# Optimization experiments

Measured on AMD Instinct MI355X. Metric: run time of the kernel, lower is better.

The kernel has to match this reference:

```python
import jax, jax.numpy as jnp
import numpy as np

HID, NH, HD = 1024, 16, 64
WIN = 512
DFF, NE, TOPK = 4096, 8, 2
B, S = 1, 2048
EPS = 1e-6


def _rope_rotation_matrix(seq_len, head_dim):
    # Block-diagonal 2x2 rotation matrices per position (standard RoPE as a fused matrix).
    pos = np.arange(seq_len, dtype=np.float64)
    inv_freq = 1.0 / (10000.0 ** (np.arange(0, head_dim, 2, dtype=np.float64) / head_dim))
    ang = pos[:, None] * inv_freq[None, :]            # [S, HD/2]
    c, s = np.cos(ang), np.sin(ang)
    R = np.zeros((seq_len, head_dim, head_dim), np.float32)
    i = np.arange(0, head_dim, 2)
    R[:, i, i] = c
    R[:, i + 1, i + 1] = c
    R[:, i, i + 1] = -s
    R[:, i + 1, i] = s
    return jnp.asarray(R)


def setup_inputs() -> dict:
    key = jax.random.key(0)
    ks = jax.random.split(key, 10)
    init = lambda k, shape, scale=0.02: (jax.random.normal(k, shape, jnp.float32) * scale)
    return {
        "x": jax.random.normal(ks[0], (B, S, HID), jnp.float32),
        "rotation_matrix": _rope_rotation_matrix(S, HD),
        "rms1_w": jnp.ones((HID,), jnp.float32),
        "wq": init(ks[1], (HID, HID)),
        "wk": init(ks[2], (HID, HID)),
        "wv": init(ks[3], (HID, HID)),
        "wo": init(ks[4], (HID, HID)),
        "rms2_w": jnp.ones((HID,), jnp.float32),
        "gate_w": init(ks[5], (HID, NE)),
        "w1": init(ks[6], (NE, HID, DFF)),
        "w2": init(ks[7], (NE, DFF, HID)),
        "w3": init(ks[8], (NE, HID, DFF)),
    }


def _rmsnorm(x, w):
    return x * jax.lax.rsqrt(jnp.mean(x * x, axis=-1, keepdims=True) + EPS) * w


def reference(x, rotation_matrix, rms1_w, wq, wk, wv, wo, rms2_w, gate_w, w1, w2, w3):
    b, s, _ = x.shape
    # --- sliding-window attention with fused RoPE rotation matrix ---
    y = _rmsnorm(x, rms1_w)
    q = (y @ wq).reshape(b, s, NH, HD).transpose(0, 2, 1, 3)  # bhsd
    k = (y @ wk).reshape(b, s, NH, HD).transpose(0, 2, 1, 3)
    v = (y @ wv).reshape(b, s, NH, HD).transpose(0, 2, 1, 3)
    q = jnp.einsum('bhsd,sde->bhse', q, rotation_matrix)
    k = jnp.einsum('bhsd,sde->bhse', k, rotation_matrix)
    scores = jnp.einsum('bhqd,bhkd->bhqk', q, k) / np.float32(np.sqrt(HD))
    idx = jnp.arange(s)
    mask = (idx[:, None] >= idx[None, :]) & (idx[:, None] - idx[None, :] < WIN)
    scores = jnp.where(mask[None, None], scores, jnp.float32(-1e9))
    att = jax.nn.softmax(scores, axis=-1)
    attn_out = jnp.einsum('bhqk,bhkd->bhqd', att, v)
    attn_out = attn_out.transpose(0, 2, 1, 3).reshape(b, s, HID) @ wo
    x = x + attn_out
    # --- MoE SwiGLU FFN with top-k routing ---
    y = _rmsnorm(x, rms2_w)
    t = y.reshape(b * s, HID)                                  # [T, D]
    logits = t @ gate_w                                        # [T, E]
    top_v, top_i = jax.lax.top_k(logits, TOPK)
    gates = jax.nn.softmax(top_v, axis=-1)                     # [T, K]
    w_full = jnp.zeros((b * s, NE), t.dtype).at[
        jnp.arange(b * s)[:, None], top_i].set(gates)          # [T, E] sparse routing weights
    h = jax.nn.silu(jnp.einsum('td,edf->etf', t, w1)) * jnp.einsum('td,edf->etf', t, w3)
    expert_out = jnp.einsum('etf,efd->etd', h, w2)             # [E, T, D]
    moe = jnp.einsum('te,etd->td', w_full, expert_out).reshape(b, s, HID)
    return x + moe
```

## Files before the change

kernel.cpp:

```cpp
#include <hip/hip_runtime.h>
#include <hip/hip_bf16.h>
#include <stdint.h>


#define S_ 2048
#define HID_ 1024
#define NH_ 16
#define HD_ 64
#define WIN_ 512
#define DFF_ 4096
#define NE_ 8

typedef unsigned short u16;
typedef __attribute__((ext_vector_type(8))) short short8;
typedef __attribute__((ext_vector_type(4))) float f32x4;

__device__ __forceinline__ u16 f2bf(float f) {
  union { float f; unsigned u; } v; v.f = f;
  unsigned r = (v.u + 0x7FFFu + ((v.u >> 16) & 1u)) >> 16;
  return (u16)r;
}
__device__ __forceinline__ float bf2f(u16 b) {
  union { unsigned u; float f; } v; v.u = ((unsigned)b) << 16;
  return v.f;
}

__device__ __forceinline__ void gload16(const void* g, void* l) {
  __builtin_amdgcn_global_load_lds(
      (const __attribute__((address_space(1))) void*)g,
      (__attribute__((address_space(3))) void*)l, 16, 0, 0);
}

template <int N>
__device__ __forceinline__ void waitcnt_vm() {
  static_assert(N == 0 || N == 4 || N == 8 || N == 12 || N == 16 || N == 24,
                "unsupported vmcnt");
  if constexpr (N == 0) asm volatile("s_waitcnt vmcnt(0)" ::: "memory");
  else if constexpr (N == 4) asm volatile("s_waitcnt vmcnt(4)" ::: "memory");
  else if constexpr (N == 8) asm volatile("s_waitcnt vmcnt(8)" ::: "memory");
  else if constexpr (N == 12) asm volatile("s_waitcnt vmcnt(12)" ::: "memory");
  else if constexpr (N == 16) asm volatile("s_waitcnt vmcnt(16)" ::: "memory");
  else if constexpr (N == 24) asm volatile("s_waitcnt vmcnt(24)" ::: "memory");
}

__global__ __launch_bounds__(256) void convT_f32_k(const float* __restrict__ W,
                                                   u16* __restrict__ WT,
                                                   int K, int N, size_t matStride) {
  __shared__ u16 t[64][72];
  const float* Wm = W + (size_t)blockIdx.z * matStride;
  u16* WTm = WT + (size_t)blockIdx.z * matStride;
  int n0 = blockIdx.x * 64, k0 = blockIdx.y * 64;
  int tid = threadIdx.x;
  int cw = (tid & 15) * 4, rr = tid >> 4;
#pragma unroll
  for (int p = 0; p < 4; ++p) {
    int r = p * 16 + rr;
    float4 v = *(const float4*)&Wm[(size_t)(k0 + r) * N + n0 + cw];
    t[cw][r] = f2bf(v.x);
    t[cw + 1][r] = f2bf(v.y);
    t[cw + 2][r] = f2bf(v.z);
    t[cw + 3][r] = f2bf(v.w);
  }
  __syncthreads();
#pragma unroll
  for (int p = 0; p < 4; ++p) {
    int n = p * 16 + rr;
    ushort4 pk = *(const ushort4*)&t[n][cw];
    *(ushort4*)&WTm[(size_t)(n0 + n) * K + k0 + cw] = pk;
  }
}

__global__ __launch_bounds__(256) void convT_qkvo_k(const float* __restrict__ wq,
                                                    const float* __restrict__ wk,
                                                    const float* __restrict__ wv,
                                                    const float* __restrict__ wo,
                                                    u16* __restrict__ outT) {
  __shared__ u16 t[64][72];
  int z = blockIdx.z;
  const float* Wm = (z == 0) ? wq : (z == 1) ? wk : (z == 2) ? wv : wo;
  u16* WTm = outT + (size_t)z * HID_ * HID_;
  int n0 = blockIdx.x * 64, k0 = blockIdx.y * 64;
  int tid = threadIdx.x;
  int cw = (tid & 15) * 4, rr = tid >> 4;
#pragma unroll
  for (int p = 0; p < 4; ++p) {
    int r = p * 16 + rr;
    float4 v = *(const float4*)&Wm[(size_t)(k0 + r) * HID_ + n0 + cw];
    t[cw][r] = f2bf(v.x);
    t[cw + 1][r] = f2bf(v.y);
    t[cw + 2][r] = f2bf(v.z);
    t[cw + 3][r] = f2bf(v.w);
  }
  __syncthreads();
#pragma unroll
  for (int p = 0; p < 4; ++p) {
    int n = p * 16 + rr;
    ushort4 pk = *(const ushort4*)&t[n][cw];
    *(ushort4*)&WTm[(size_t)(n0 + n) * HID_ + k0 + cw] = pk;
  }
}

__global__ __launch_bounds__(256) void convT_u16_k(const u16* __restrict__ W,
                                                   u16* __restrict__ WT,
                                                   int K, int N, size_t matStride) {
  __shared__ u16 t[64][66];
  const u16* Wm = W + (size_t)blockIdx.z * matStride;
  u16* WTm = WT + (size_t)blockIdx.z * matStride;
  int n0 = blockIdx.x * 64, k0 = blockIdx.y * 64;
  int tid = threadIdx.x;
  int c2 = (tid & 31) * 2, rr = tid >> 5;
#pragma unroll
  for (int it = 0; it < 8; ++it) {
    int r = it * 8 + rr;
    unsigned vv = *(const unsigned*)&Wm[(size_t)(k0 + r) * N + n0 + c2];
    t[c2][r] = (u16)vv;
    t[c2 + 1][r] = (u16)(vv >> 16);
  }
  __syncthreads();
#pragma unroll
  for (int it = 0; it < 8; ++it) {
    int n = it * 8 + rr;
    unsigned pk = (unsigned)t[n][c2] | ((unsigned)t[n][c2 + 1] << 16);
    *(unsigned*)&WTm[(size_t)(n0 + n) * K + k0 + c2] = pk;
  }
}

__global__ __launch_bounds__(256) void rope_tab_k(const float* __restrict__ rot,
                                                  float* __restrict__ cost,
                                                  float* __restrict__ sint) {
  int id = blockIdx.x * 256 + threadIdx.x;
  if (id >= S_ * 32) return;
  int s = id >> 5, j = id & 31;
  cost[id] = rot[(size_t)s * 4096 + (size_t)(2 * j) * 64 + 2 * j];
  sint[id] = rot[(size_t)s * 4096 + (size_t)(2 * j + 1) * 64 + 2 * j];
}

__global__ __launch_bounds__(256) void rms1_k(const float* __restrict__ x,
                                              const float* __restrict__ rw,
                                              u16* __restrict__ y) {
  int row = blockIdx.x, tid = threadIdx.x;
  const float4 v = *(const float4*)&x[(size_t)row * HID_ + tid * 4];
  float ss = v.x * v.x + v.y * v.y + v.z * v.z + v.w * v.w;
#pragma unroll
  for (int o = 32; o; o >>= 1) ss += __shfl_xor(ss, o);
  __shared__ float red[4];
  if ((tid & 63) == 0) red[tid >> 6] = ss;
  __syncthreads();
  float rstd = rsqrtf((red[0] + red[1] + red[2] + red[3]) * (1.f / HID_) + 1e-6f);
  const float4 w4 = *(const float4*)&rw[tid * 4];
  ushort4 o4;
  o4.x = f2bf(v.x * rstd * w4.x);
  o4.y = f2bf(v.y * rstd * w4.y);
  o4.z = f2bf(v.z * rstd * w4.z);
  o4.w = f2bf(v.w * rstd * w4.w);
  *(ushort4*)&y[(size_t)row * HID_ + tid * 4] = o4;
}

__global__ __launch_bounds__(256) void rms2_gate_k(const float* __restrict__ x2,
                                                   const float* __restrict__ rw,
                                                   const float* __restrict__ gw,
                                                   u16* __restrict__ y2,
                                                   float* __restrict__ logits) {
  int row = blockIdx.x, tid = threadIdx.x;
  int wv = tid >> 6, ln = tid & 63;
  const float4 v = *(const float4*)&x2[(size_t)row * HID_ + tid * 4];
  float ss = v.x * v.x + v.y * v.y + v.z * v.z + v.w * v.w;
#pragma unroll
  for (int o = 32; o; o >>= 1) ss += __shfl_xor(ss, o);
  __shared__ float red[4];
  __shared__ float lred[4][8];
  if (ln == 0) red[wv] = ss;
  __syncthreads();
  float rstd = rsqrtf((red[0] + red[1] + red[2] + red[3]) * (1.f / HID_) + 1e-6f);
  const float4 w4 = *(const float4*)&rw[tid * 4];
  float yv[4];
  yv[0] = v.x * rstd * w4.x; yv[1] = v.y * rstd * w4.y;
  yv[2] = v.z * rstd * w4.z; yv[3] = v.w * rstd * w4.w;
  ushort4 o4;
  o4.x = f2bf(yv[0]); o4.y = f2bf(yv[1]); o4.z = f2bf(yv[2]); o4.w = f2bf(yv[3]);
  *(ushort4*)&y2[(size_t)row * HID_ + tid * 4] = o4;
  float le[8] = {0, 0, 0, 0, 0, 0, 0, 0};
  int d0 = tid * 4;
#pragma unroll
  for (int j = 0; j < 4; ++j) {
    const float* grow = &gw[(size_t)(d0 + j) * NE_];
#pragma unroll
    for (int e = 0; e < 8; ++e) le[e] += yv[j] * grow[e];
  }
#pragma unroll
  for (int e = 0; e < 8; ++e) {
    float t = le[e];
#pragma unroll
    for (int o = 32; o; o >>= 1) t += __shfl_xor(t, o);
    le[e] = t;
  }
  if (ln == 0)
#pragma unroll
    for (int e = 0; e < 8; ++e) lred[wv][e] = le[e];
  __syncthreads();
  if (tid < 8)
    logits[(size_t)row * NE_ + tid] =
        lred[0][tid] + lred[1][tid] + lred[2][tid] + lred[3][tid];
}

__global__ __launch_bounds__(1024) void route_k(const float* __restrict__ logits,
                                                int* __restrict__ topi,
                                                float* __restrict__ topg,
                                                int* __restrict__ counts,
                                                int* __restrict__ ebase,
                                                int* __restrict__ slot_token,
                                                int* __restrict__ slot_of) {
  __shared__ int cnt[8], bas[8], rnk[8];
  int tid = threadIdx.x;
  if (tid < 8) { cnt[tid] = 0; rnk[tid] = 0; }
  __syncthreads();
  int e0[2], e1[2];
  float g0[2], g1[2];
#pragma unroll
  for (int s = 0; s < 2; ++s) {
    int t = tid * 2 + s;
    const float* lg = &logits[(size_t)t * NE_];
    float v0 = -1e30f; int i0 = 0;
#pragma unroll
    for (int e = 0; e < 8; ++e) {
      float x = lg[e];
      if (x > v0) { v0 = x; i0 = e; }
    }
    float v1 = -1e30f; int i1 = 0;
#pragma unroll
    for (int e = 0; e < 8; ++e) {
      if (e == i0) continue;
      float x = lg[e];
      if (x > v1) { v1 = x; i1 = e; }
    }
    float ex = __expf(v1 - v0);
    e0[s] = i0; e1[s] = i1;
    g0[s] = 1.f / (1.f + ex);
    g1[s] = ex / (1.f + ex);
    topi[t * 2] = i0; topi[t * 2 + 1] = i1;
    topg[t * 2] = g0[s]; topg[t * 2 + 1] = g1[s];
    atomicAdd(&cnt[i0], 1);
    atomicAdd(&cnt[i1], 1);
  }
  __syncthreads();
  if (tid == 0) {
    int s = 0;
    for (int e = 0; e < 8; ++e) { bas[e] = s; s += cnt[e]; }
  }
  __syncthreads();
#pragma unroll
  for (int s = 0; s < 2; ++s) {
    int t = tid * 2 + s;
    int p0 = bas[e0[s]] + atomicAdd(&rnk[e0[s]], 1);
    int p1 = bas[e1[s]] + atomicAdd(&rnk[e1[s]], 1);
    slot_token[p0] = t; slot_token[p1] = t;
    slot_of[t * 2] = p0; slot_of[t * 2 + 1] = p1;
  }
  if (tid < 8) { counts[tid] = cnt[tid]; ebase[tid] = bas[tid]; }
}

template <int MODE, int SLOTS>
__global__ __launch_bounds__(256, (SLOTS <= 3 ? 3 : (SLOTS <= 5 ? 2 : 1)))
void gemm3_k(
    const u16* __restrict__ A, const u16* __restrict__ B0,
    const u16* __restrict__ B1, const u16* __restrict__ B2, int K,
    const int* __restrict__ ecnt, const int* __restrict__ ebase,
    const float* __restrict__ cost, const float* __restrict__ sint,
    const float* __restrict__ xres, float* __restrict__ outf,
    u16* __restrict__ o0, u16* __restrict__ o1, u16* __restrict__ o2) {
  constexpr int WVM = 4 * (SLOTS - 2);
  __shared__ alignas(16) char smem[SLOTS * 16384];

  int n0 = blockIdx.x * 128, m0 = blockIdx.y * 128;
  int cnt = 0, base = 0;
  const u16* Bp;
  u16* outb = o0;
  int rope = 0;
  if constexpr (MODE == 0) {
    int z = blockIdx.z;
    Bp = (z == 0) ? B0 : (z == 1) ? B1 : B2;
    outb = (z == 0) ? o0 : (z == 1) ? o1 : o2;
    rope = (z < 2) ? 1 : 0;
  } else if constexpr (MODE == 1) {
    Bp = B0;
  } else {
    int e = blockIdx.z;
    cnt = ecnt[e]; base = ebase[e];
    if (m0 >= cnt) return;
    Bp = B0 + (size_t)e * HID_ * DFF_;
  }

  int tid = threadIdx.x, w = tid >> 6, l = tid & 63, lo = l & 15, g = l >> 4;
  int wm = w >> 1, wn = w & 1;
  int KT = K >> 5;
  size_t rb = (size_t)K * 2;

  int lrow = l >> 2, lu = l & 3;
  const char* pA[2];
  const char* pB[2];
  int ldOff[2];
#pragma unroll
  for (int j = 0; j < 2; ++j) {
    int rA = j * 64 + w * 16 + lrow;
    int swz = (lu ^ ((rA >> 1) & 3)) << 4;
    size_t arow;
    if constexpr (MODE == 3) {
      arow = (size_t)(base + min(m0 + rA, cnt - 1));
    } else {
      arow = (size_t)(m0 + rA);
    }
    pA[j] = (const char*)A + arow * rb + swz;
    pB[j] = (const char*)Bp + (size_t)(n0 + rA) * rb + swz;
    ldOff[j] = (j * 64 + w * 16) * 64;
  }

  auto stage = [&](int t) {
    char* s = smem + (t % SLOTS) * 16384;
    size_t kb = (size_t)t * 64;
    gload16(pA[0] + kb, s + ldOff[0]);
    gload16(pA[1] + kb, s + ldOff[1]);
    gload16(pB[0] + kb, s + 8192 + ldOff[0]);
    gload16(pB[1] + kb, s + 8192 + ldOff[1]);
  };

  f32x4 acc[4][4];
#pragma unroll
  for (int i = 0; i < 4; ++i)
#pragma unroll
    for (int j = 0; j < 4; ++j) acc[i][j] = (f32x4){0.f, 0.f, 0.f, 0.f};

#pragma unroll
  for (int s = 0; s < SLOTS - 1; ++s) stage(min(s, KT - 1));
  waitcnt_vm<WVM>();
  __builtin_amdgcn_s_barrier();

  for (int t = 0; t < KT; ++t) {
    char* s = smem + (t % SLOTS) * 16384;
    stage(min(t + SLOTS - 1, KT - 1));
    short8 afr[4], bfr[4];
#pragma unroll
    for (int mi = 0; mi < 4; ++mi) {
      int r = wm * 64 + mi * 16 + lo;
      afr[mi] = *(const short8*)(s + r * 64 + ((g ^ ((r >> 1) & 3)) << 4));
    }
#pragma unroll
    for (int ni = 0; ni < 4; ++ni) {
      int r = wn * 64 + ni * 16 + lo;
      bfr[ni] = *(const short8*)(s + 8192 + r * 64 + ((g ^ ((r >> 1) & 3)) << 4));
    }
    asm volatile("s_waitcnt lgkmcnt(0)" ::: "memory");
    __builtin_amdgcn_s_setprio(1);
#pragma unroll
    for (int mi = 0; mi < 4; ++mi)
#pragma unroll
      for (int ni = 0; ni < 4; ++ni)
        acc[mi][ni] = __builtin_amdgcn_mfma_f32_16x16x32_bf16(afr[mi], bfr[ni], acc[mi][ni], 0, 0, 0);
    __builtin_amdgcn_s_setprio(0);
    if (t + 1 < KT)
      waitcnt_vm<WVM>();
    else
      waitcnt_vm<0>();
    __builtin_amdgcn_s_barrier();
  }
  asm volatile("s_waitcnt vmcnt(0) lgkmcnt(0)" ::: "memory");

#pragma unroll
  for (int mi = 0; mi < 4; ++mi) {
    int lr = wm * 64 + mi * 16 + g * 4;
#pragma unroll
    for (int ni = 0; ni < 4; ++ni) {
      int c = n0 + wn * 64 + ni * 16 + lo;
#pragma unroll
      for (int r = 0; r < 4; ++r) {
        float v = acc[mi][ni][r];
        if constexpr (MODE == 0) {
          int row = m0 + lr + r;
          float p = __shfl_xor(v, 1);
          if (rope) {
            int dd = c & 63;
            float co = cost[(size_t)row * 32 + (dd >> 1)];
            float si = sint[(size_t)row * 32 + (dd >> 1)];
            v = (dd & 1) ? (co * v - si * p) : (co * v + si * p);
          }
          outb[((size_t)(c >> 6) * S_ + row) * HD_ + (c & 63)] = f2bf(v);
        } else if constexpr (MODE == 1) {
          int row = m0 + lr + r;
          outf[(size_t)row * HID_ + c] = v + xres[(size_t)row * HID_ + c];
        } else {
          int m = m0 + lr + r;
          if (m < cnt) outb[(size_t)(base + m) * HID_ + c] = f2bf(v);
        }
      }
    }
  }
}

template <int TPB, int MODE>
__global__ __launch_bounds__(TPB, 2) void gemm5_k(
    const u16* __restrict__ A, const u16* __restrict__ B0,
    const u16* __restrict__ B1, int K, const int* __restrict__ ecnt,
    const int* __restrict__ ebase, const int* __restrict__ slot_token,
    u16* __restrict__ o0, u16* __restrict__ o1) {
  constexpr int NW = TPB / 64;
  constexpr int WN = NW / 2;
  constexpr int BM = TPB / 2;
  constexpr int MROW = BM / 2;
  constexpr int MI = MROW / 16;
  constexpr int MH = MI / 2;
  constexpr int ABYTES = BM * 128;
  __shared__ alignas(16) char smem[ABYTES * 4];
  char* ldsA = smem;
  char* ldsB = smem + 2 * ABYTES;

  int n0 = blockIdx.x * BM, m0 = blockIdx.y * BM;
  int cnt = 0, base = 0;
  const u16* Bp;
  u16* outb;
  {
    int e = blockIdx.z >> 1, mat = blockIdx.z & 1;
    cnt = ecnt[e]; base = ebase[e];
    if (m0 >= cnt) return;
    Bp = (mat ? B1 : B0) + (size_t)e * DFF_ * HID_;
    outb = mat ? o1 : o0;
  }

  int tid = threadIdx.x, w = tid >> 6, l = tid & 63, lo = l & 15, g = l >> 4;
  int wm = w / WN, wn = w % WN;
  int KT = K >> 6;
  size_t rb = (size_t)K * 2;

  int lrow = l >> 3, lu = l & 7;
  const char* pA[4];
  const char* pB[4];
  int ldOff[4];
#pragma unroll
  for (int j = 0; j < 4; ++j) {
    int rA = j * (BM / 4) + w * 8 + lrow;
    int swz = (lu ^ (rA & 7)) << 4;
    size_t arow = (size_t)slot_token[base + min(m0 + rA, cnt - 1)];
    pA[j] = (const char*)A + arow * rb + swz;
    pB[j] = (const char*)Bp + (size_t)(n0 + rA) * rb + swz;
    ldOff[j] = (j * (BM / 4) + w * 8) * 128;
  }

  auto stA = [&](int t, int j) {
    gload16(pA[j] + (size_t)t * 128, ldsA + (t & 1) * ABYTES + ldOff[j]);
  };
  auto stB = [&](int t, int j) {
    gload16(pB[j] + (size_t)t * 128, ldsB + (t & 1) * ABYTES + ldOff[j]);
  };
  auto rdA = [&](int d, int mi, int kh) {
    int row = wm * MROW + mi * 16 + lo;
    return *(const short8*)(ldsA + d * ABYTES + row * 128 +
                            (((kh * 4 + g) ^ (row & 7)) << 4));
  };
  auto rdB = [&](int d, int ni, int kh) {
    int row = wn * 64 + ni * 16 + lo;
    return *(const short8*)(ldsB + d * ABYTES + row * 128 +
                            (((kh * 4 + g) ^ (row & 7)) << 4));
  };

  f32x4 acc[MI][4];
#pragma unroll
  for (int i = 0; i < MI; ++i)
#pragma unroll
    for (int j = 0; j < 4; ++j) acc[i][j] = (f32x4){0.f, 0.f, 0.f, 0.f};

  stB(0, 0); stB(0, 1); stB(0, 2); stB(0, 3);
  stA(0, 0); stA(0, 2);
  stA(0, 1); stA(0, 3);
  {
    int t1 = min(1, KT - 1);
    stA(t1, 0); stA(t1, 2);
  }
  asm volatile("s_waitcnt vmcnt(4)" ::: "memory");
  __builtin_amdgcn_s_barrier();

  for (int t = 0; t < KT; ++t) {
    int d = t & 1;
    int tn = min(t + 1, KT - 1);
    int tn2 = min(t + 2, KT - 1);
    short8 afr[MH], bfr[4];
    stB(tn, 0); stB(tn, 1);
#pragma unroll
    for (int i = 0; i < MH; ++i) afr[i] = rdA(d, i, 0);
#pragma unroll
    for (int n = 0; n < 4; ++n) bfr[n] = rdB(d, n, 0);
    asm volatile("s_waitcnt lgkmcnt(0)" ::: "memory");
    __builtin_amdgcn_s_setprio(1);
#pragma unroll
    for (int i = 0; i < MH; ++i)
#pragma unroll
      for (int n = 0; n < 4; ++n)
        acc[i][n] = __builtin_amdgcn_mfma_f32_16x16x32_bf16(afr[i], bfr[n], acc[i][n], 0, 0, 0);
    __builtin_amdgcn_s_setprio(0);
    asm volatile("s_waitcnt vmcnt(4)" ::: "memory");
    __builtin_amdgcn_s_barrier();
    stB(tn, 2); stB(tn, 3);
#pragma unroll
    for (int i = 0; i < MH; ++i) afr[i] = rdA(d, MH + i, 0);
    asm volatile("s_waitcnt lgkmcnt(0)" ::: "memory");
    __builtin_amdgcn_s_setprio(1);
#pragma unroll
    for (int i = 0; i < MH; ++i)
#pragma unroll
      for (int n = 0; n < 4; ++n)
        acc[MH + i][n] = __builtin_amdgcn_mfma_f32_16x16x32_bf16(afr[i], bfr[n], acc[MH + i][n], 0, 0, 0);
    __builtin_amdgcn_s_setprio(0);
    __builtin_amdgcn_s_barrier();
    stA(tn, 1); stA(tn, 3);
#pragma unroll
    for (int i = 0; i < MH; ++i) afr[i] = rdA(d, i, 1);
#pragma unroll
    for (int n = 0; n < 4; ++n) bfr[n] = rdB(d, n, 1);
    asm volatile("s_waitcnt lgkmcnt(0)" ::: "memory");
    __builtin_amdgcn_s_setprio(1);
#pragma unroll
    for (int i = 0; i < MH; ++i)
#pragma unroll
      for (int n = 0; n < 4; ++n)
        acc[i][n] = __builtin_amdgcn_mfma_f32_16x16x32_bf16(afr[i], bfr[n], acc[i][n], 0, 0, 0);
    __builtin_amdgcn_s_setprio(0);
    __builtin_amdgcn_s_barrier();
    stA(tn2, 0); stA(tn2, 2);
#pragma unroll
    for (int i = 0; i < MH; ++i) afr[i] = rdA(d, MH + i, 1);
    asm volatile("s_waitcnt lgkmcnt(0)" ::: "memory");
    __builtin_amdgcn_s_setprio(1);
#pragma unroll
    for (int i = 0; i < MH; ++i)
#pragma unroll
      for (int n = 0; n < 4; ++n)
        acc[MH + i][n] = __builtin_amdgcn_mfma_f32_16x16x32_bf16(afr[i], bfr[n], acc[MH + i][n], 0, 0, 0);
    __builtin_amdgcn_s_setprio(0);
    asm volatile("s_waitcnt vmcnt(4)" ::: "memory");
    __builtin_amdgcn_s_barrier();
  }
  asm volatile("s_waitcnt vmcnt(0) lgkmcnt(0)" ::: "memory");

#pragma unroll
  for (int mi = 0; mi < MI; ++mi) {
    int lr = wm * MROW + mi * 16 + g * 4;
#pragma unroll
    for (int ni = 0; ni < 4; ++ni) {
      int c = n0 + wn * 64 + ni * 16 + lo;
#pragma unroll
      for (int r = 0; r < 4; ++r) {
        int m = m0 + lr + r;
        if (m < cnt) outb[(size_t)(base + m) * DFF_ + c] = f2bf(acc[mi][ni][r]);
      }
    }
  }
}

__global__ __launch_bounds__(256) void swiglu_k(u16* __restrict__ h1,
                                                const u16* __restrict__ h3) {
  size_t i = ((size_t)blockIdx.x * 256 + threadIdx.x) * 8;
  short8 a = *(const short8*)(h1 + i);
  short8 b = *(const short8*)(h3 + i);
  short8 o;
#pragma unroll
  for (int j = 0; j < 8; ++j) {
    float x = bf2f((u16)a[j]), y = bf2f((u16)b[j]);
    float s = x / (1.f + __expf(-x));
    o[j] = (short)f2bf(s * y);
  }
  *(short8*)(h1 + i) = o;
}

__global__ __launch_bounds__(256) void attn_k(const u16* __restrict__ qh,
                                              const u16* __restrict__ kh,
                                              const u16* __restrict__ vht,
                                              u16* __restrict__ attn) {
  int qt = blockIdx.x, h = blockIdx.y;
  int tid = threadIdx.x, w = tid >> 6, l = tid & 63, lo = l & 15, g = l >> 4;
  __shared__ alignas(16) char Ks[8192];
  __shared__ alignas(16) char Vs[8192];
  __shared__ alignas(16) char Ps[8192];
  char* Pw = Ps + w * 2048;
  int q0 = qt * 64, qw = q0 + w * 16;
  const u16* qhh = qh + ((size_t)h * S_ + qw) * HD_;
  short8 bq0 = *(const short8*)(qhh + lo * 64 + g * 8);
  short8 bq1 = *(const short8*)(qhh + lo * 64 + 32 + g * 8);
  int q = qw + lo;
  float m_run = -1e30f, l_run = 0.f;
  f32x4 o[4];
#pragma unroll
  for (int i = 0; i < 4; ++i) o[i] = (f32x4){0.f, 0.f, 0.f, 0.f};
  int kt0 = max(0, q0 - (WIN_ - 1)) >> 6;
  for (int kt = kt0; kt <= qt; ++kt) {
    int kb = kt * 64;
    {
      int r0 = w * 16 + (l >> 3), r1 = r0 + 8;
      int uu = l & 7;
      short8 k0v = *(const short8*)(kh + ((size_t)h * S_ + kb + r0) * HD_ + uu * 8);
      short8 k1v = *(const short8*)(kh + ((size_t)h * S_ + kb + r1) * HD_ + uu * 8);
      short8 v0v = *(const short8*)(vht + ((size_t)h * HD_ + r0) * S_ + kb + uu * 8);
      short8 v1v = *(const short8*)(vht + ((size_t)h * HD_ + r1) * S_ + kb + uu * 8);
      *(short8*)(Ks + r0 * 128 + ((uu ^ (r0 & 7)) << 4)) = k0v;
      *(short8*)(Ks + r1 * 128 + ((uu ^ (r1 & 7)) << 4)) = k1v;
      *(short8*)(Vs + r0 * 128 + ((uu ^ (r0 & 7)) << 4)) = v0v;
      *(short8*)(Vs + r1 * 128 + ((uu ^ (r1 & 7)) << 4)) = v1v;
    }
    __syncthreads();
    f32x4 st[4];
#pragma unroll
    for (int kf = 0; kf < 4; ++kf) {
      int key = kf * 16 + lo;
      short8 a0 = *(const short8*)(Ks + key * 128 + ((g ^ (key & 7)) << 4));
      short8 a1 = *(const short8*)(Ks + key * 128 + (((4 + g) ^ (key & 7)) << 4));
      f32x4 z = (f32x4){0.f, 0.f, 0.f, 0.f};
      z = __builtin_amdgcn_mfma_f32_16x16x32_bf16(a0, bq0, z, 0, 0, 0);
      z = __builtin_amdgcn_mfma_f32_16x16x32_bf16(a1, bq1, z, 0, 0, 0);
      st[kf] = z;
    }
    float p[16];
    float tmax = -1e30f;
#pragma unroll
    for (int kf = 0; kf < 4; ++kf)
#pragma unroll
      for (int r = 0; r < 4; ++r) {
        int key = kb + kf * 16 + g * 4 + r;
        float s = st[kf][r] * 0.125f;
        bool okm = (key <= q) && (q - key < WIN_);
        s = okm ? s : -1e30f;
        p[kf * 4 + r] = s;
        tmax = fmaxf(tmax, s);
      }
    tmax = fmaxf(tmax, __shfl_xor(tmax, 16));
    tmax = fmaxf(tmax, __shfl_xor(tmax, 32));
    float m_new = fmaxf(m_run, tmax);
    float corr = __expf(m_run - m_new);
    float tsum = 0.f;
#pragma unroll
    for (int i = 0; i < 16; ++i) {
      float pe = (p[i] > -1e29f) ? __expf(p[i] - m_new) : 0.f;
      p[i] = pe;
      tsum += pe;
    }
    tsum += __shfl_xor(tsum, 16);
    tsum += __shfl_xor(tsum, 32);
    l_run = l_run * corr + tsum;
    m_run = m_new;
#pragma unroll
    for (int kf = 0; kf < 4; ++kf)
#pragma unroll
      for (int pr = 0; pr < 2; ++pr) {
        int keyloc = kf * 16 + g * 4 + pr * 2;
        unsigned pk = (unsigned)f2bf(p[kf * 4 + pr * 2]) |
                      ((unsigned)f2bf(p[kf * 4 + pr * 2 + 1]) << 16);
        *(unsigned*)(Pw + lo * 128 + (((keyloc >> 3) ^ (lo & 7)) << 4) +
                     (keyloc & 7) * 2) = pk;
      }
    float c0 = __shfl(corr, g * 4 + 0), c1 = __shfl(corr, g * 4 + 1);
    float c2 = __shfl(corr, g * 4 + 2), c3 = __shfl(corr, g * 4 + 3);
#pragma unroll
    for (int nf = 0; nf < 4; ++nf) {
      o[nf][0] *= c0; o[nf][1] *= c1; o[nf][2] *= c2; o[nf][3] *= c3;
    }
    short8 ap0 = *(const short8*)(Pw + lo * 128 + ((g ^ (lo & 7)) << 4));
    short8 ap1 = *(const short8*)(Pw + lo * 128 + (((4 + g) ^ (lo & 7)) << 4));
#pragma unroll
    for (int nf = 0; nf < 4; ++nf) {
      int d = nf * 16 + lo;
      short8 v0 = *(const short8*)(Vs + d * 128 + ((g ^ (d & 7)) << 4));
      short8 v1 = *(const short8*)(Vs + d * 128 + (((4 + g) ^ (d & 7)) << 4));
      o[nf] = __builtin_amdgcn_mfma_f32_16x16x32_bf16(ap0, v0, o[nf], 0, 0, 0);
      o[nf] = __builtin_amdgcn_mfma_f32_16x16x32_bf16(ap1, v1, o[nf], 0, 0, 0);
    }
    __syncthreads();
  }
  float linv = 1.f / l_run;
  float i0 = __shfl(linv, g * 4 + 0), i1 = __shfl(linv, g * 4 + 1);
  float i2 = __shfl(linv, g * 4 + 2), i3 = __shfl(linv, g * 4 + 3);
#pragma unroll
  for (int nf = 0; nf < 4; ++nf) {
    int d = nf * 16 + lo;
    attn[(size_t)(qw + g * 4 + 0) * HID_ + h * HD_ + d] = f2bf(o[nf][0] * i0);
    attn[(size_t)(qw + g * 4 + 1) * HID_ + h * HD_ + d] = f2bf(o[nf][1] * i1);
    attn[(size_t)(qw + g * 4 + 2) * HID_ + h * HD_ + d] = f2bf(o[nf][2] * i2);
    attn[(size_t)(qw + g * 4 + 3) * HID_ + h * HD_ + d] = f2bf(o[nf][3] * i3);
  }
}

__global__ __launch_bounds__(256) void combine_k(float* __restrict__ out,
                                                 const u16* __restrict__ eo,
                                                 const int* __restrict__ slot_of,
                                                 const float* __restrict__ topg) {
  int row = blockIdx.x, tid = threadIdx.x;
  int d0 = tid * 4;
  int p0 = slot_of[row * 2], p1 = slot_of[row * 2 + 1];
  float g0 = topg[row * 2], g1 = topg[row * 2 + 1];
  float4 cur = *(float4*)&out[(size_t)row * HID_ + d0];
  ushort4 ea = *(const ushort4*)&eo[(size_t)p0 * HID_ + d0];
  ushort4 eb = *(const ushort4*)&eo[(size_t)p1 * HID_ + d0];
  cur.x += g0 * bf2f(ea.x) + g1 * bf2f(eb.x);
  cur.y += g0 * bf2f(ea.y) + g1 * bf2f(eb.y);
  cur.z += g0 * bf2f(ea.z) + g1 * bf2f(eb.z);
  cur.w += g0 * bf2f(ea.w) + g1 * bf2f(eb.w);
  *(float4*)&out[(size_t)row * HID_ + d0] = cur;
}

extern "C" void kernel_launch(void* const* d_in, const int* in_sizes, int n_in,
                              void* d_out, int out_size, void* d_ws,
                              size_t ws_size, hipStream_t stream) {
  const float* x = (const float*)d_in[0];
  const float* rot = (const float*)d_in[1];
  const float* r1w = (const float*)d_in[2];
  const float* wq = (const float*)d_in[3];
  const float* wk = (const float*)d_in[4];
  const float* wv = (const float*)d_in[5];
  const float* wo = (const float*)d_in[6];
  const float* r2w = (const float*)d_in[7];
  const float* gw = (const float*)d_in[8];
  const float* w1 = (const float*)d_in[9];
  const float* w2 = (const float*)d_in[10];
  const float* w3 = (const float*)d_in[11];
  float* out = (float*)d_out;

  char* ws = (char*)d_ws;
  size_t off = 0;
  auto alloc = [&](size_t bytes) {
    char* p = ws + off;
    off += (bytes + 255) & ~(size_t)255;
    return p;
  };
  const size_t MB4 = (size_t)S_ * HID_ * 2;
  u16* wqkvoT = (u16*)alloc((size_t)4 * HID_ * HID_ * 2);
  u16* wqT = wqkvoT;
  u16* wkT = wqkvoT + (size_t)HID_ * HID_;
  u16* wvT = wqkvoT + (size_t)2 * HID_ * HID_;
  u16* woT = wqkvoT + (size_t)3 * HID_ * HID_;
  u16* w1T = (u16*)alloc((size_t)NE_ * DFF_ * HID_ * 2);
  u16* w3T = (u16*)alloc((size_t)NE_ * DFF_ * HID_ * 2);
  u16* w2T = (u16*)alloc((size_t)NE_ * HID_ * DFF_ * 2);
  char* uni = alloc((size_t)2 * S_ * DFF_ * 2);
  u16* ybf = (u16*)(uni);
  u16* qh = (u16*)(uni + MB4);
  u16* kh = (u16*)(uni + 2 * MB4);
  u16* vh = (u16*)(uni + 3 * MB4);
  u16* vht = (u16*)(uni + 4 * MB4);
  u16* attnb = (u16*)(uni + 5 * MB4);
  u16* h3 = (u16*)uni;
  u16* y2bf = (u16*)alloc(MB4);
  u16* h1 = (u16*)alloc((size_t)2 * S_ * DFF_ * 2);
  u16* eo = (u16*)alloc((size_t)2 * S_ * HID_ * 2);
  float* cost = (float*)alloc((size_t)S_ * 32 * 4);
  float* sint = (float*)alloc((size_t)S_ * 32 * 4);
  float* logits = (float*)alloc((size_t)S_ * NE_ * 4);
  int* topi = (int*)alloc((size_t)S_ * 2 * 4);
  float* topg = (float*)alloc((size_t)S_ * 2 * 4);
  int* ints = (int*)alloc(256);
  int* counts = ints;
  int* ebase = ints + 8;
  int* slot_token = (int*)alloc((size_t)2 * S_ * 4);
  int* slot_of = (int*)alloc((size_t)S_ * 2 * 4);
  (void)ws_size; (void)in_sizes; (void)n_in; (void)out_size;

  convT_qkvo_k<<<dim3(16, 16, 4), 256, 0, stream>>>(wq, wk, wv, wo, wqkvoT);
  convT_f32_k<<<dim3(64, 16, 8), 256, 0, stream>>>(w1, w1T, HID_, DFF_, (size_t)HID_ * DFF_);
  convT_f32_k<<<dim3(64, 16, 8), 256, 0, stream>>>(w3, w3T, HID_, DFF_, (size_t)HID_ * DFF_);
  convT_f32_k<<<dim3(16, 64, 8), 256, 0, stream>>>(w2, w2T, DFF_, HID_, (size_t)DFF_ * HID_);

  rope_tab_k<<<dim3(256), 256, 0, stream>>>(rot, cost, sint);
  rms1_k<<<dim3(S_), 256, 0, stream>>>(x, r1w, ybf);

  gemm3_k<0, 5><<<dim3(8, 16, 3), 256, 0, stream>>>(
      ybf, wqT, wkT, wvT, HID_, nullptr, nullptr, cost, sint, nullptr,
      nullptr, qh, kh, vh);
  convT_u16_k<<<dim3(1, 32, 16), 256, 0, stream>>>(vh, vht, S_, HD_, (size_t)S_ * HD_);

  attn_k<<<dim3(32, 16), 256, 0, stream>>>(qh, kh, vht, attnb);

  gemm3_k<1, 5><<<dim3(8, 16, 1), 256, 0, stream>>>(
      attnb, woT, nullptr, nullptr, HID_, nullptr, nullptr, nullptr, nullptr,
      x, out, nullptr, nullptr, nullptr);

  rms2_gate_k<<<dim3(S_), 256, 0, stream>>>(out, r2w, gw, y2bf, logits);
  route_k<<<dim3(1), 1024, 0, stream>>>(logits, topi, topg, counts, ebase,
                                        slot_token, slot_of);

  gemm5_k<512, 2><<<dim3(16, 8, 16), 512, 0, stream>>>(
      y2bf, w1T, w3T, HID_, counts, ebase, slot_token, h1, h3);
  swiglu_k<<<dim3(8192), 256, 0, stream>>>(h1, h3);
  gemm3_k<3, 8><<<dim3(8, 16, 8), 256, 0, stream>>>(
      h1, w2T, nullptr, nullptr, DFF_, counts, ebase, nullptr, nullptr,
      nullptr, nullptr, eo, nullptr, nullptr);
  combine_k<<<dim3(S_), 256, 0, stream>>>(out, eo, slot_of, topg);
}
```

Measured before the change: 435.4 us.

## Split-K the MoE down-projection GEMM into two halves with fp32 partials

The expert down-projection GEMM now runs as a split-K kernel. Each expert's DFF reduction is divided into two halves across blockIdx.z, and each half writes fp32 partial results into a reused scratch buffer. The combine kernel sums both partials before applying the gate weights. This doubles the block count so that sparsely populated experts fill more CUs, and it uses fewer pipeline slots so more blocks fit per CU. The cost is extra fp32 partial traffic, plus one more read per slot in the combine step.

```diff
diff --git a/kernel.cpp b/kernel.cpp
--- a/kernel.cpp
+++ b/kernel.cpp
@@ -272,9 +272,10 @@
   __shared__ alignas(16) char smem[SLOTS * 16384];
 
   int n0 = blockIdx.x * 128, m0 = blockIdx.y * 128;
-  int cnt = 0, base = 0;
+  int cnt = 0, base = 0, kc = 0;
   const u16* Bp;
   u16* outb = o0;
+  float* pout = outf;
   int rope = 0;
   if constexpr (MODE == 0) {
     int z = blockIdx.z;
@@ -283,6 +284,13 @@
     rope = (z < 2) ? 1 : 0;
   } else if constexpr (MODE == 1) {
     Bp = B0;
+  } else if constexpr (MODE == 4) {
+    int e = blockIdx.z >> 1;
+    kc = blockIdx.z & 1;
+    cnt = ecnt[e]; base = ebase[e];
+    if (m0 >= cnt) return;
+    Bp = B0 + (size_t)e * HID_ * DFF_;
+    pout = outf + (size_t)kc * ((size_t)2 * S_ * HID_);
   } else {
     int e = blockIdx.z;
     cnt = ecnt[e]; base = ebase[e];
@@ -293,7 +301,8 @@
   int tid = threadIdx.x, w = tid >> 6, l = tid & 63, lo = l & 15, g = l >> 4;
   int wm = w >> 1, wn = w & 1;
   int KT = K >> 5;
-  size_t rb = (size_t)K * 2;
+  size_t rb = (MODE == 4) ? (size_t)DFF_ * 2 : (size_t)K * 2;
+  size_t kcoff = (MODE == 4) ? (size_t)kc * (size_t)(DFF_ / 2) * 2 : 0;
 
   int lrow = l >> 2, lu = l & 3;
   const char* pA[2];
@@ -304,13 +313,13 @@
     int rA = j * 64 + w * 16 + lrow;
     int swz = (lu ^ ((rA >> 1) & 3)) << 4;
     size_t arow;
-    if constexpr (MODE == 3) {
+    if constexpr (MODE == 3 || MODE == 4) {
       arow = (size_t)(base + min(m0 + rA, cnt - 1));
     } else {
       arow = (size_t)(m0 + rA);
     }
-    pA[j] = (const char*)A + arow * rb + swz;
-    pB[j] = (const char*)Bp + (size_t)(n0 + rA) * rb + swz;
+    pA[j] = (const char*)A + arow * rb + kcoff + swz;
+    pB[j] = (const char*)Bp + (size_t)(n0 + rA) * rb + kcoff + swz;
     ldOff[j] = (j * 64 + w * 16) * 64;
   }
 
@@ -386,6 +395,9 @@
         } else if constexpr (MODE == 1) {
           int row = m0 + lr + r;
           outf[(size_t)row * HID_ + c] = v + xres[(size_t)row * HID_ + c];
+        } else if constexpr (MODE == 4) {
+          int m = m0 + lr + r;
+          if (m < cnt) pout[(size_t)(base + m) * HID_ + c] = v;
         } else {
           int m = m0 + lr + r;
           if (m < cnt) outb[(size_t)(base + m) * HID_ + c] = f2bf(v);
@@ -684,20 +696,23 @@
 }
 
 __global__ __launch_bounds__(256) void combine_k(float* __restrict__ out,
-                                                 const u16* __restrict__ eo,
+                                                 const float* __restrict__ part,
                                                  const int* __restrict__ slot_of,
                                                  const float* __restrict__ topg) {
   int row = blockIdx.x, tid = threadIdx.x;
   int d0 = tid * 4;
+  const size_t PS = (size_t)2 * S_ * HID_;
   int p0 = slot_of[row * 2], p1 = slot_of[row * 2 + 1];
   float g0 = topg[row * 2], g1 = topg[row * 2 + 1];
   float4 cur = *(float4*)&out[(size_t)row * HID_ + d0];
-  ushort4 ea = *(const ushort4*)&eo[(size_t)p0 * HID_ + d0];
-  ushort4 eb = *(const ushort4*)&eo[(size_t)p1 * HID_ + d0];
-  cur.x += g0 * bf2f(ea.x) + g1 * bf2f(eb.x);
-  cur.y += g0 * bf2f(ea.y) + g1 * bf2f(eb.y);
-  cur.z += g0 * bf2f(ea.z) + g1 * bf2f(eb.z);
-  cur.w += g0 * bf2f(ea.w) + g1 * bf2f(eb.w);
+  float4 a0 = *(const float4*)&part[(size_t)p0 * HID_ + d0];
+  float4 a1 = *(const float4*)&part[PS + (size_t)p0 * HID_ + d0];
+  float4 b0 = *(const float4*)&part[(size_t)p1 * HID_ + d0];
+  float4 b1 = *(const float4*)&part[PS + (size_t)p1 * HID_ + d0];
+  cur.x += g0 * (a0.x + a1.x) + g1 * (b0.x + b1.x);
+  cur.y += g0 * (a0.y + a1.y) + g1 * (b0.y + b1.y);
+  cur.z += g0 * (a0.z + a1.z) + g1 * (b0.z + b1.z);
+  cur.w += g0 * (a0.w + a1.w) + g1 * (b0.w + b1.w);
   *(float4*)&out[(size_t)row * HID_ + d0] = cur;
 }
 
@@ -742,9 +757,9 @@
   u16* vht = (u16*)(uni + 4 * MB4);
   u16* attnb = (u16*)(uni + 5 * MB4);
   u16* h3 = (u16*)uni;
+  float* partials = (float*)uni;
   u16* y2bf = (u16*)alloc(MB4);
   u16* h1 = (u16*)alloc((size_t)2 * S_ * DFF_ * 2);
-  u16* eo = (u16*)alloc((size_t)2 * S_ * HID_ * 2);
   float* cost = (float*)alloc((size_t)S_ * 32 * 4);
   float* sint = (float*)alloc((size_t)S_ * 32 * 4);
   float* logits = (float*)alloc((size_t)S_ * NE_ * 4);
@@ -783,8 +798,8 @@
   gemm5_k<512, 2><<<dim3(16, 8, 16), 512, 0, stream>>>(
       y2bf, w1T, w3T, HID_, counts, ebase, slot_token, h1, h3);
   swiglu_k<<<dim3(8192), 256, 0, stream>>>(h1, h3);
-  gemm3_k<3, 8><<<dim3(8, 16, 8), 256, 0, stream>>>(
-      h1, w2T, nullptr, nullptr, DFF_, counts, ebase, nullptr, nullptr,
-      nullptr, nullptr, eo, nullptr, nullptr);
-  combine_k<<<dim3(S_), 256, 0, stream>>>(out, eo, slot_of, topg);
-}
+  gemm3_k<4, 4><<<dim3(8, 16, 16), 256, 0, stream>>>(
+      h1, w2T, nullptr, nullptr, DFF_ / 2, counts, ebase, nullptr, nullptr,
+      nullptr, partials, nullptr, nullptr, nullptr);
+  combine_k<<<dim3(S_), 256, 0, stream>>>(out, partials, slot_of, topg);
+}
```

Result: faster. 417.7 us (-4.1%).
